# Kernel optimization log

Hardware: AMD Instinct MI355X
Metric: run time of the kernel (lower is better)

## Reference

```python
import jax, jax.numpy as jnp
import numpy as np

N_HEADS = 4

def layernorm(x, g, b):
    m = jnp.mean(x, -1, keepdims=True)
    v = jnp.var(x, -1, keepdims=True)
    return (x - m) / jnp.sqrt(v + 1e-5) * g + b

def conv1d(x, w, b, pad):
    y = jax.lax.conv_general_dilated(x, w, (1,), [(pad, pad)], dimension_numbers=('NCH', 'OIH', 'NCH'))
    return y + b[None, :, None]

def bn_eval(x, g, b, m, v):
    return (x - m[None, :, None]) / jnp.sqrt(v[None, :, None] + 1e-5) * g[None, :, None] + b[None, :, None]

def maxpool(x, k):
    return jax.lax.reduce_window(x, -jnp.inf, jax.lax.max, (1, 1, k), (1, 1, k), 'VALID')

def _forward(x, conv1_w, conv1_b, bn1_g, bn1_b, bn1_m, bn1_v, conv2_w, conv2_b, bn2_g, bn2_b, bn2_m, bn2_v, adj_prior, log_weights, gat_n1_g, gat_n1_b, gat_qkv_w, gat_qkv_b, gat_out_w, gat_out_b, gat_n2_g, gat_n2_b, gat_f1_w, gat_f1_b, gat_f2_w, gat_f2_b, gatn_g, gatn_b, gru_wih, gru_whh, gru_bih, gru_bhh, gate_w, gate_b):
    B, C, T = x.shape
    D = conv2_w.shape[0]
    dk = D // N_HEADS
    scale = dk ** -0.5
    # --- per-channel temporal CNN: (B,C,T) -> (B,C,T',D), T' = T//16 ---
    h = x.reshape(B * C, 1, T)
    h = maxpool(jax.nn.gelu(bn_eval(conv1d(h, conv1_w, conv1_b, 3), bn1_g, bn1_b, bn1_m, bn1_v), approximate=False), 4)
    h = maxpool(jax.nn.gelu(bn_eval(conv1d(h, conv2_w, conv2_b, 2), bn2_g, bn2_b, bn2_m, bn2_v), approximate=False), 4)
    Tp = h.shape[-1]
    h = jnp.transpose(h, (0, 2, 1)).reshape(B, C, Tp, D)
    # --- spectral dynamic adjacency ---
    h_avg = h.mean(axis=2)                                   # (B,C,D)
    hc = h_avg - h_avg.mean(-1, keepdims=True)
    hn = hc / (jnp.linalg.norm(hc, axis=-1, keepdims=True) + 1e-8)
    feat_corr = jnp.einsum('bcd,bed->bce', hn, hn)
    Xp = jnp.abs(jnp.fft.rfft(x, axis=-1))
    Xn = Xp / (jnp.linalg.norm(Xp, axis=-1, keepdims=True) + 1e-8)
    spec_coh = jnp.einsum('bcf,bef->bce', Xn, Xn)
    prior = (adj_prior + adj_prior.T)[None]
    w = jax.nn.softmax(log_weights)
    adj = w[0] * feat_corr + w[1] * spec_coh + w[2] * prior  # (B,C,C)
    # --- GAT stack over the C-node channel graph at every timestep ---
    ht = jnp.transpose(h, (0, 2, 1, 3)).reshape(B * Tp, C, D)
    adj_t = jnp.broadcast_to(adj[:, None], (B, Tp, C, C)).reshape(B * Tp, C, C)
    L = gat_qkv_w.shape[0]
    for l in range(L):
        hn1 = layernorm(ht, gat_n1_g[l], gat_n1_b[l])
        qkv = (hn1 @ gat_qkv_w[l].T + gat_qkv_b[l]).reshape(B * Tp, C, 3, N_HEADS, dk)
        q = jnp.moveaxis(qkv[:, :, 0], 1, 2)                 # (N,H,C,dk)
        k = jnp.moveaxis(qkv[:, :, 1], 1, 2)
        v = jnp.moveaxis(qkv[:, :, 2], 1, 2)
        attn = jnp.einsum('nhqd,nhkd->nhqk', q, k) * scale + adj_t[:, None]
        attn = jax.nn.softmax(attn, axis=-1)                 # dropout off (eval)
        out = jnp.einsum('nhqk,nhkd->nhqd', attn, v)
        out = jnp.moveaxis(out, 1, 2).reshape(B * Tp, C, D)
        ht = ht + out @ gat_out_w[l].T + gat_out_b[l]
        hn2 = layernorm(ht, gat_n2_g[l], gat_n2_b[l])
        ffn = jax.nn.gelu(hn2 @ gat_f1_w[l].T + gat_f1_b[l], approximate=False) @ gat_f2_w[l].T + gat_f2_b[l]
        ht = ht + ffn
    ht = layernorm(ht, gatn_g, gatn_b)
    hs = ht.reshape(B, Tp, C, D).transpose(0, 2, 1, 3).reshape(B * C, Tp, D)
    # --- bidirectional GRU (1 layer), final hidden states only ---
    G = gru_whh.shape[-1]
    def gru_last(xs, wih, whh, bih, bhh):
        def step(hprev, xt):
            gi = xt @ wih.T + bih
            gh = hprev @ whh.T + bhh
            ir, iz, inn = jnp.split(gi, 3, -1)
            hr, hz, hnn = jnp.split(gh, 3, -1)
            r = jax.nn.sigmoid(ir + hr)
            z = jax.nn.sigmoid(iz + hz)
            n = jnp.tanh(inn + r * hnn)
            hnew = (1.0 - z) * n + z * hprev
            return hnew, None
        h0 = jnp.zeros((xs.shape[0], G), xs.dtype)
        hl, _ = jax.lax.scan(step, h0, jnp.moveaxis(xs, 1, 0))
        return hl
    h_f = gru_last(hs, gru_wih[0], gru_whh[0], gru_bih[0], gru_bhh[0])
    h_b = gru_last(hs[:, ::-1], gru_wih[1], gru_whh[1], gru_bih[1], gru_bhh[1])
    h_out = jnp.concatenate([h_f, h_b], -1).reshape(B, C, 2 * G)
    # --- channel-attention readout ---
    gate = jax.nn.sigmoid(h_out @ gate_w.T + gate_b)         # (B,C,1)
    readout = (h_out * gate).sum(1) / (gate.sum(1) + 1e-8)   # (B,2G)
    return readout, adj, gate

def setup_inputs() -> dict:
    key = jax.random.key(0)
    ks = iter(jax.random.split(key, 64))
    B, C, T = 32, 16, 4096
    D, L, G = 64, 2, 64
    def rn(shape, s=0.08):
        return jax.random.normal(next(ks), shape, jnp.float32) * s
    return dict(
        x=jax.random.normal(next(ks), (B, C, T), jnp.float32),
        conv1_w=rn((32, 1, 7), 0.2), conv1_b=rn((32,)),
        bn1_g=jnp.ones((32,)), bn1_b=jnp.zeros((32,)), bn1_m=jnp.zeros((32,)), bn1_v=jnp.ones((32,)),
        conv2_w=rn((D, 32, 5), 0.1), conv2_b=rn((D,)),
        bn2_g=jnp.ones((D,)), bn2_b=jnp.zeros((D,)), bn2_m=jnp.zeros((D,)), bn2_v=jnp.ones((D,)),
        adj_prior=rn((C, C), 0.1), log_weights=jnp.zeros((3,)),
        gat_n1_g=jnp.ones((L, D)), gat_n1_b=jnp.zeros((L, D)),
        gat_qkv_w=rn((L, 3 * D, D)), gat_qkv_b=jnp.zeros((L, 3 * D)),
        gat_out_w=rn((L, D, D)), gat_out_b=jnp.zeros((L, D)),
        gat_n2_g=jnp.ones((L, D)), gat_n2_b=jnp.zeros((L, D)),
        gat_f1_w=rn((L, 2 * D, D)), gat_f1_b=jnp.zeros((L, 2 * D)),
        gat_f2_w=rn((L, D, 2 * D)), gat_f2_b=jnp.zeros((L, D)),
        gatn_g=jnp.ones((D,)), gatn_b=jnp.zeros((D,)),
        gru_wih=rn((2, 3 * G, D)), gru_whh=rn((2, 3 * G, G)),
        gru_bih=jnp.zeros((2, 3 * G)), gru_bhh=jnp.zeros((2, 3 * G)),
        gate_w=rn((1, 2 * G)), gate_b=jnp.zeros((1,)),
    )

def reference(x, conv1_w, conv1_b, bn1_g, bn1_b, bn1_m, bn1_v, conv2_w, conv2_b, bn2_g, bn2_b, bn2_m, bn2_v, adj_prior, log_weights, gat_n1_g, gat_n1_b, gat_qkv_w, gat_qkv_b, gat_out_w, gat_out_b, gat_n2_g, gat_n2_b, gat_f1_w, gat_f1_b, gat_f2_w, gat_f2_b, gatn_g, gatn_b, gru_wih, gru_whh, gru_bih, gru_bhh, gate_w, gate_b):
    return _forward(x, conv1_w, conv1_b, bn1_g, bn1_b, bn1_m, bn1_v, conv2_w, conv2_b, bn2_g, bn2_b, bn2_m, bn2_v, adj_prior, log_weights, gat_n1_g, gat_n1_b, gat_qkv_w, gat_qkv_b, gat_out_w, gat_out_b, gat_n2_g, gat_n2_b, gat_f1_w, gat_f1_b, gat_f2_w, gat_f2_b, gatn_g, gatn_b, gru_wih, gru_whh, gru_bih, gru_bhh, gate_w, gate_b)
```

## Files before the change

kernel.cpp:

```cpp
#include <hip/hip_runtime.h>
#include <hip/hip_bf16.h>
#include <math.h>

typedef __hip_bfloat16 bf16;
typedef unsigned short ushort_t;
typedef __attribute__((ext_vector_type(8))) short short8;
typedef __attribute__((ext_vector_type(4))) float f32x4;

__device__ __forceinline__ float b2f(bf16 v) { return __bfloat162float(v); }
__device__ __forceinline__ bf16 f2b(float v) { return __float2bfloat16(v); }
__device__ __forceinline__ float sigmoidf_(float x) { return 1.0f / (1.0f + __expf(-x)); }

__device__ __forceinline__ float geluf(float x) {
    float z = x * 0.70710678118654752f;
    float az = fabsf(z);
    float t = 1.0f / (1.0f + 0.3275911f * az);
    float poly = ((((1.061405429f * t - 1.453152027f) * t + 1.421413741f) * t
                   - 0.284496736f) * t + 0.254829592f) * t;
    float erfa = 1.0f - poly * __expf(-z * z);
    float er = (z < 0.f) ? -erfa : erfa;
    return 0.5f * x * (1.0f + er);
}

__device__ __forceinline__ unsigned pack2bf(float a, float b) {
    unsigned ua = __float_as_uint(a); ua = (ua + 0x7FFFu + ((ua >> 16) & 1u)) >> 16;
    unsigned ub = __float_as_uint(b); ub = (ub + 0x7FFFu + ((ub >> 16) & 1u)) >> 16;
    return ua | (ub << 16);
}
__device__ __forceinline__ ushort_t f2bu(float v) {
    unsigned u = __float_as_uint(v);
    u = (u + 0x7FFFu + ((u >> 16) & 1u)) >> 16;
    return (ushort_t)u;
}

__global__ __launch_bounds__(256) void k_detect(const unsigned* __restrict__ x, int* __restrict__ flag)
{
    __shared__ int cnt;
    if (threadIdx.x == 0) cnt = 0;
    __syncthreads();
    unsigned u = x[threadIdx.x] & 0xFFFFu;
    float f = __uint_as_float(u << 16);
    float a = fabsf(f);
    int sane = (f == 0.0f) || (a > 1e-8f && a < 1e4f);
    atomicAdd(&cnt, sane);
    __syncthreads();
    if (threadIdx.x == 0) *flag = (cnt >= 160) ? 1 : 0;
}

struct InPtrs { const void* p[35]; };
struct InOffs { int off[35]; int sz[35]; };

__global__ __launch_bounds__(256) void k_convert(InPtrs P, InOffs O, int total,
                                                 const int* __restrict__ flag,
                                                 float* __restrict__ cvt)
{
    int idx = blockIdx.x * 256 + threadIdx.x;
    if (idx >= total) return;
    int isb = *flag;
    float v = 0.f;
#pragma unroll 1
    for (int s = 0; s < 35; s++) {
        int rel = idx - O.off[s];
        if (rel >= 0 && rel < O.sz[s]) {
            v = isb ? b2f(((const bf16*)P.p[s])[rel]) : ((const float*)P.p[s])[rel];
            break;
        }
    }
    cvt[idx] = v;
}

__global__ __launch_bounds__(256) void k_pack(const float* __restrict__ qw, const float* __restrict__ ow,
                                              const float* __restrict__ f1w, const float* __restrict__ f2w,
                                              const float* __restrict__ gwih, const float* __restrict__ gwhh,
                                              const float* __restrict__ c2w,
                                              unsigned* __restrict__ dst)
{
    int i = blockIdx.x * 256 + threadIdx.x;
    if (i >= 62464) return;
    if (i >= 57344) {
        int j0 = (i - 57344) * 2;
        int tap = j0 >> 11, rem = j0 & 2047;
        int d = rem >> 5, ic = rem & 31;
        dst[i] = pack2bf(c2w[d * 160 + ic * 5 + tap], c2w[d * 160 + (ic + 1) * 5 + tap]);
        return;
    }
    const float* s; int rel;
    if (i < 12288)      { s = qw;   rel = i; }
    else if (i < 16384) { s = ow;   rel = i - 12288; }
    else if (i < 24576) { s = f1w;  rel = i - 16384; }
    else if (i < 32768) { s = f2w;  rel = i - 24576; }
    else if (i < 45056) { s = gwih; rel = i - 32768; }
    else                { s = gwhh; rel = i - 45056; }
    dst[i] = pack2bf(s[2 * rel], s[2 * rel + 1]);
}

__global__ __launch_bounds__(256) void k_front(
    const float* __restrict__ x,
    const float* __restrict__ c1w, const float* __restrict__ c1b,
    const float* __restrict__ bn1g, const float* __restrict__ bn1b, const float* __restrict__ bn1m, const float* __restrict__ bn1v,
    const float* __restrict__ c2b,
    const float* __restrict__ bn2g, const float* __restrict__ bn2b, const float* __restrict__ bn2m, const float* __restrict__ bn2v,
    const ushort_t* __restrict__ w2pk,
    float* __restrict__ h_main, float* __restrict__ Xn, float* __restrict__ hnf)
{
    __shared__ float smem[9984];
    int t = threadIdx.x;
    if (blockIdx.x >= 512) {
        float* re = smem;
        float* im = smem + 4096;
        float* red = smem + 8192;
        int bc = blockIdx.x - 512;
        const float* xr = x + (size_t)bc * 4096;
        for (int i = t; i < 4096; i += 256) {
            int r = __brev((unsigned)i) >> 20;
            re[r] = xr[i];
            im[r] = 0.f;
        }
        __syncthreads();
        for (int s = 1; s <= 12; s++) {
            int half = 1 << (s - 1);
            float ang = -6.283185307179586f / (float)(1 << s);
            for (int m = t; m < 2048; m += 256) {
                int j = m & (half - 1);
                int pos = ((m >> (s - 1)) << s) | j;
                float sn, cs;
                __sincosf(ang * (float)j, &sn, &cs);
                float ur = re[pos], ui = im[pos];
                float vr = re[pos + half], vi = im[pos + half];
                float tr = vr * cs - vi * sn;
                float ti = vr * sn + vi * cs;
                re[pos] = ur + tr; im[pos] = ui + ti;
                re[pos + half] = ur - tr; im[pos + half] = ui - ti;
            }
            __syncthreads();
        }
        float mag[9];
        float ss = 0.f;
        int cnt = 0;
        for (int f = t; f <= 2048; f += 256) {
            float m2 = re[f] * re[f] + im[f] * im[f];
            mag[cnt++] = sqrtf(m2);
            ss += m2;
        }
        for (int off = 32; off; off >>= 1) ss += __shfl_xor(ss, off, 64);
        if ((t & 63) == 0) red[t >> 6] = ss;
        __syncthreads();
        float tot = red[0] + red[1] + red[2] + red[3];
        float inv = 1.0f / (sqrtf(tot) + 1e-8f);
        cnt = 0;
        for (int f = t; f <= 2048; f += 256) Xn[(size_t)bc * 2049 + f] = mag[cnt++] * inv;
        return;
    }
    float* ubuf = smem;
    ushort_t* h1t = (ushort_t*)(smem + 4352);
    float* A2s = smem + 9552;
    float* B2s = smem + 9616;
    float* hsum = smem + 9680;
    int bc = blockIdx.x;
    int l = t & 63, w = t >> 6;
    int lo = l & 15, quad = l >> 4;

    if (t < 64) {
        float s = bn2g[t] * rsqrtf(bn2v[t] + 1e-5f);
        A2s[t] = s; B2s[t] = (c2b[t] - bn2m[t]) * s + bn2b[t];
    }
    int icp = t & 15;
    float w1r[2][7], A1r[2], B1r[2];
#pragma unroll
    for (int s = 0; s < 2; s++) {
        int ic = icp * 2 + s;
#pragma unroll
        for (int k = 0; k < 7; k++) w1r[s][k] = c1w[ic * 7 + k];
        float sc = bn1g[ic] * rsqrtf(bn1v[ic] + 1e-5f);
        A1r[s] = sc; B1r[s] = (c1b[ic] - bn1m[ic]) * sc + bn1b[ic];
    }
    short8 Afr[4][5];
#pragma unroll
    for (int dt = 0; dt < 4; dt++)
#pragma unroll
        for (int tap = 0; tap < 5; tap++)
            Afr[dt][tap] = *(const short8*)(w2pk + ((tap * 64 + dt * 16 + lo) * 32 + quad * 8));

    const float* xrow = x + (size_t)bc * 4096;
    float rs = 0.f;
    int dd = t & 63, pg = t >> 6;
    for (int tile = 0; tile < 4; tile++) {
        int X0 = 1024 * tile - 11;
        for (int i = t; i < 1056; i += 256) {
            int g = X0 + i;
            ubuf[i] = (g >= 0 && g < 4096) ? xrow[g] : 0.0f;
        }
        __syncthreads();
        for (int pos = (t >> 4); pos < 260; pos += 16) {
            const float4* xw = (const float4*)&ubuf[4 * pos];
            float4 fa = xw[0], fb = xw[1], fc = xw[2];
            float xv[12] = {fa.x, fa.y, fa.z, fa.w, fb.x, fb.y, fb.z, fb.w,
                            fc.x, fc.y, fc.z, fc.w};
            int t1pg = tile * 256 + pos - 2;
            bool ok = (t1pg >= 0 && t1pg < 1024);
            float res[2];
#pragma unroll
            for (int s = 0; s < 2; s++) {
                float a0 = 0.f, a1 = 0.f, a2 = 0.f, a3 = 0.f;
#pragma unroll
                for (int k = 0; k < 7; k++) {
                    float wv = w1r[s][k];
                    a0 += xv[k] * wv;     a1 += xv[k + 1] * wv;
                    a2 += xv[k + 2] * wv; a3 += xv[k + 3] * wv;
                }
                float A = A1r[s], B = B1r[s];
                a0 = a0 * A + B; a1 = a1 * A + B; a2 = a2 * A + B; a3 = a3 * A + B;
                float mx = fmaxf(fmaxf(a0, a1), fmaxf(a2, a3));
                float mn = fminf(fminf(a0, a1), fminf(a2, a3));
                res[s] = ok ? fmaxf(geluf(mx), geluf(mn)) : 0.0f;
            }
            ((unsigned*)h1t)[pos * 20 + icp] = pack2bf(res[0], res[1]);
        }
        __syncthreads();
        float* houtile = ubuf;
#pragma unroll
        for (int ni = 0; ni < 4; ni++) {
            int nt = w * 4 + ni;
            short8 bfr[5];
#pragma unroll
            for (int tap = 0; tap < 5; tap++)
                bfr[tap] = *(const short8*)&h1t[(nt * 16 + lo + tap) * 40 + quad * 8];
#pragma unroll
            for (int dt = 0; dt < 4; dt++) {
                f32x4 acc = {0.f, 0.f, 0.f, 0.f};
#pragma unroll
                for (int tap = 0; tap < 5; tap++)
                    acc = __builtin_amdgcn_mfma_f32_16x16x32_bf16(Afr[dt][tap], bfr[tap], acc, 0, 0, 0);
                const float4 a2 = *(const float4*)&A2s[dt * 16 + quad * 4];
                const float4 b2 = *(const float4*)&B2s[dt * 16 + quad * 4];
                float a2a[4] = {a2.x, a2.y, a2.z, a2.w};
                float b2a[4] = {b2.x, b2.y, b2.z, b2.w};
#pragma unroll
                for (int r = 0; r < 4; r++) {
                    float v = acc[r] * a2a[r] + b2a[r];
                    float o1 = __shfl_xor(v, 1);
                    float mx = fmaxf(v, o1), mn = fminf(v, o1);
                    float mx2 = __shfl_xor(mx, 2), mn2 = __shfl_xor(mn, 2);
                    mx = fmaxf(mx, mx2); mn = fminf(mn, mn2);
                    float res = fmaxf(geluf(mx), geluf(mn));
                    if ((lo & 3) == 0)
                        houtile[(nt * 4 + (lo >> 2)) * 68 + dt * 16 + quad * 4 + r] = res;
                }
            }
        }
        __syncthreads();
#pragma unroll
        for (int i = 0; i < 16; i++) rs += ubuf[(pg * 16 + i) * 68 + dd];
        float* dst = h_main + (size_t)bc * 16384 + tile * 4096;
        for (int i = t * 4; i < 4096; i += 1024) {
            float4 v = *(const float4*)&ubuf[(i >> 6) * 68 + (i & 63)];
            *(float4*)&dst[i] = v;
        }
        __syncthreads();
    }
    hsum[t] = rs;
    __syncthreads();
    if (t < 64) {
        float avg = (hsum[t] + hsum[64 + t] + hsum[128 + t] + hsum[192 + t]) * (1.0f / 256.0f);
        float tot = avg;
        for (int off = 32; off; off >>= 1) tot += __shfl_xor(tot, off, 64);
        float hc = avg - tot * (1.0f / 64.0f);
        float sq = hc * hc;
        for (int off = 32; off; off >>= 1) sq += __shfl_xor(sq, off, 64);
        hnf[bc * 64 + t] = hc / (sqrtf(sq) + 1e-8f);
    }
}

__global__ __launch_bounds__(256) void k_adj(
    const float* __restrict__ Xn, const float* __restrict__ hnf,
    const float* __restrict__ prior, const float* __restrict__ logw,
    float* __restrict__ adjw, void* __restrict__ out, const int* __restrict__ flag)
{
    __shared__ float xt[16][257];
    __shared__ float hh[16 * 64];
    int b = blockIdx.x, t = threadIdx.x;
    int c = t >> 4, e = t & 15;
    for (int i = t; i < 1024; i += 256) hh[i] = hnf[b * 1024 + i];
    __syncthreads();
    float fc = 0.f;
    for (int d = 0; d < 64; d++) fc += hh[c * 64 + d] * hh[e * 64 + d];
    float sc = 0.f;
    const float* Xb = Xn + (size_t)b * 16 * 2049;
    for (int f0 = 0; f0 < 2048; f0 += 256) {
        __syncthreads();
        for (int i = t; i < 16 * 256; i += 256) {
            int rr = i >> 8, ff = i & 255;
            xt[rr][ff] = Xb[rr * 2049 + f0 + ff];
        }
        __syncthreads();
        for (int ff = 0; ff < 256; ff++) sc += xt[c][ff] * xt[e][ff];
    }
    sc += Xb[c * 2049 + 2048] * Xb[e * 2049 + 2048];
    float l0 = logw[0], l1 = logw[1], l2 = logw[2];
    float mx = fmaxf(l0, fmaxf(l1, l2));
    float e0 = __expf(l0 - mx), e1 = __expf(l1 - mx), e2 = __expf(l2 - mx);
    float isum = 1.0f / (e0 + e1 + e2);
    float pr = prior[c * 16 + e] + prior[e * 16 + c];
    float v = (e0 * fc + e1 * sc + e2 * pr) * isum;
    adjw[b * 256 + t] = v;
    if (*flag) ((bf16*)out)[4096 + b * 256 + t] = f2b(v);
    else       ((float*)out)[4096 + b * 256 + t] = v;
}

__device__ __forceinline__ void ln_wave(const float (*ht)[68], ushort_t (*out)[72],
                                        const float* __restrict__ g, const float* __restrict__ bp,
                                        int quad, int lo)
{
    float v[16];
    const float4* row = (const float4*)(&ht[lo][quad * 16]);
#pragma unroll
    for (int i = 0; i < 4; i++) {
        float4 a = row[i];
        v[4 * i] = a.x; v[4 * i + 1] = a.y; v[4 * i + 2] = a.z; v[4 * i + 3] = a.w;
    }
    float s = 0.f;
#pragma unroll
    for (int i = 0; i < 16; i++) s += v[i];
    s += __shfl_xor(s, 16); s += __shfl_xor(s, 32);
    float mean = s * (1.0f / 64.0f);
    float q = 0.f;
#pragma unroll
    for (int i = 0; i < 16; i++) { float d = v[i] - mean; q += d * d; }
    q += __shfl_xor(q, 16); q += __shfl_xor(q, 32);
    float rstd = rsqrtf(q * (1.0f / 64.0f) + 1e-5f);
    const float4* gp = (const float4*)(g + quad * 16);
    const float4* bb4 = (const float4*)(bp + quad * 16);
    unsigned* orow = (unsigned*)(&out[lo][quad * 16]);
#pragma unroll
    for (int i = 0; i < 4; i++) {
        float4 gg = gp[i], bb = bb4[i];
        float o0 = (v[4 * i] - mean) * rstd * gg.x + bb.x;
        float o1 = (v[4 * i + 1] - mean) * rstd * gg.y + bb.y;
        float o2 = (v[4 * i + 2] - mean) * rstd * gg.z + bb.z;
        float o3 = (v[4 * i + 3] - mean) * rstd * gg.w + bb.w;
        orow[2 * i] = pack2bf(o0, o1);
        orow[2 * i + 1] = pack2bf(o2, o3);
    }
}

__global__ __launch_bounds__(256) void k_gat(
    const float* __restrict__ hm, const float* __restrict__ adjw,
    const ushort_t* __restrict__ wpk,
    const float* __restrict__ qb_, const float* __restrict__ ob_,
    const float* __restrict__ f1b_, const float* __restrict__ f2b_,
    const float* __restrict__ n1g_, const float* __restrict__ n1b_,
    const float* __restrict__ n2g_, const float* __restrict__ n2b_,
    const float* __restrict__ gng, const float* __restrict__ gnb,
    ushort_t* __restrict__ hmb)
{
    __shared__ float htw_all[4][16][68];
    __shared__ ushort_t hnw_all[4][16][72];
    __shared__ ushort_t qkb_all[4][16][200];
    __shared__ ushort_t pb_all[4][16][72];
    __shared__ ushort_t vt_all[4][64][24];
    int t = threadIdx.x;
    int w = t >> 6, l = t & 63;
    int quad = l >> 4, lo = l & 15;
    int n = blockIdx.x * 4 + w;
    int b = n >> 8, tp = n & 255;
    float (*htw)[68] = htw_all[w];
    ushort_t (*hnw)[72] = hnw_all[w];
    ushort_t (*qkb)[200] = qkb_all[w];
    ushort_t (*pb)[72] = pb_all[w];
    ushort_t (*vt)[24] = vt_all[w];
    const float* src = hm + (size_t)b * 16 * 16384 + (size_t)tp * 64;
#pragma unroll
    for (int c = 0; c < 16; c++) htw[c][l] = src[(size_t)c * 16384 + l];
    float adjr[4];
#pragma unroll
    for (int r = 0; r < 4; r++) adjr[r] = adjw[b * 256 + (quad * 4 + r) * 16 + lo];

    for (int layer = 0; layer < 2; layer++) {
        const ushort_t* wq  = wpk + layer * 12288;
        const ushort_t* wo  = wpk + 24576 + layer * 4096;
        const ushort_t* wf1 = wpk + 32768 + layer * 8192;
        const ushort_t* wf2 = wpk + 49152 + layer * 8192;
        const float* qb = qb_ + layer * 192;
        const float* ob = ob_ + layer * 64;
        const float* f1b = f1b_ + layer * 128;
        const float* f2b = f2b_ + layer * 64;

        ln_wave(htw, hnw, n1g_ + layer * 64, n1b_ + layer * 64, quad, lo);

        short8 a0 = *(const short8*)&hnw[lo][quad * 8];
        short8 a1 = *(const short8*)&hnw[lo][32 + quad * 8];
#pragma unroll
        for (int nt = 0; nt < 12; nt++) {
            const ushort_t* wr = wq + (nt * 16 + lo) * 64 + quad * 8;
            short8 b0 = *(const short8*)wr;
            short8 b1 = *(const short8*)(wr + 32);
            f32x4 acc = {0.f, 0.f, 0.f, 0.f};
            acc = __builtin_amdgcn_mfma_f32_16x16x32_bf16(a0, b0, acc, 0, 0, 0);
            acc = __builtin_amdgcn_mfma_f32_16x16x32_bf16(a1, b1, acc, 0, 0, 0);
            float bias = qb[nt * 16 + lo];
            if (nt < 8) {
#pragma unroll
                for (int r = 0; r < 4; r++) qkb[quad * 4 + r][nt * 16 + lo] = f2bu(acc[r] + bias);
            } else {
#pragma unroll
                for (int r = 0; r < 4; r++) vt[(nt - 8) * 16 + lo][quad * 4 + r] = f2bu(acc[r] + bias);
            }
        }

        short8 zf = {0, 0, 0, 0, 0, 0, 0, 0};
#pragma unroll
        for (int h = 0; h < 4; h++) {
            short8 qf = zf, kf = zf;
            if (quad < 2) {
                qf = *(const short8*)&qkb[lo][h * 16 + quad * 8];
                kf = *(const short8*)&qkb[lo][64 + h * 16 + quad * 8];
            }
            f32x4 s4 = {0.f, 0.f, 0.f, 0.f};
            s4 = __builtin_amdgcn_mfma_f32_16x16x32_bf16(qf, kf, s4, 0, 0, 0);
#pragma unroll
            for (int r = 0; r < 4; r++) {
                float sv = s4[r] * 0.25f + adjr[r];
                float mx = sv;
                mx = fmaxf(mx, __shfl_xor(mx, 1));
                mx = fmaxf(mx, __shfl_xor(mx, 2));
                mx = fmaxf(mx, __shfl_xor(mx, 4));
                mx = fmaxf(mx, __shfl_xor(mx, 8));
                float e = __expf(sv - mx);
                float sm = e;
                sm += __shfl_xor(sm, 1);
                sm += __shfl_xor(sm, 2);
                sm += __shfl_xor(sm, 4);
                sm += __shfl_xor(sm, 8);
                pb[quad * 4 + r][h * 16 + lo] = f2bu(e / sm);
            }
        }
#pragma unroll
        for (int h = 0; h < 4; h++) {
            short8 pf = zf, vf = zf;
            if (quad < 2) {
                pf = *(const short8*)&pb[lo][h * 16 + quad * 8];
                vf = *(const short8*)&vt[h * 16 + lo][quad * 8];
            }
            f32x4 oc = {0.f, 0.f, 0.f, 0.f};
            oc = __builtin_amdgcn_mfma_f32_16x16x32_bf16(pf, vf, oc, 0, 0, 0);
#pragma unroll
            for (int r = 0; r < 4; r++) qkb[quad * 4 + r][h * 16 + lo] = f2bu(oc[r]);
        }
        short8 pa0 = *(const short8*)&qkb[lo][quad * 8];
        short8 pa1 = *(const short8*)&qkb[lo][32 + quad * 8];
#pragma unroll
        for (int nt = 0; nt < 4; nt++) {
            const ushort_t* wr = wo + (nt * 16 + lo) * 64 + quad * 8;
            short8 b0 = *(const short8*)wr;
            short8 b1 = *(const short8*)(wr + 32);
            f32x4 acc = {0.f, 0.f, 0.f, 0.f};
            acc = __builtin_amdgcn_mfma_f32_16x16x32_bf16(pa0, b0, acc, 0, 0, 0);
            acc = __builtin_amdgcn_mfma_f32_16x16x32_bf16(pa1, b1, acc, 0, 0, 0);
            float bias = ob[nt * 16 + lo];
#pragma unroll
            for (int r = 0; r < 4; r++) htw[quad * 4 + r][nt * 16 + lo] += acc[r] + bias;
        }
        ln_wave(htw, hnw, n2g_ + layer * 64, n2b_ + layer * 64, quad, lo);
        short8 fa0 = *(const short8*)&hnw[lo][quad * 8];
        short8 fa1 = *(const short8*)&hnw[lo][32 + quad * 8];
#pragma unroll
        for (int nt = 0; nt < 8; nt++) {
            const ushort_t* wr = wf1 + (nt * 16 + lo) * 64 + quad * 8;
            short8 b0 = *(const short8*)wr;
            short8 b1 = *(const short8*)(wr + 32);
            f32x4 acc = {0.f, 0.f, 0.f, 0.f};
            acc = __builtin_amdgcn_mfma_f32_16x16x32_bf16(fa0, b0, acc, 0, 0, 0);
            acc = __builtin_amdgcn_mfma_f32_16x16x32_bf16(fa1, b1, acc, 0, 0, 0);
            float bias = f1b[nt * 16 + lo];
#pragma unroll
            for (int r = 0; r < 4; r++) qkb[quad * 4 + r][nt * 16 + lo] = f2bu(geluf(acc[r] + bias));
        }
        short8 ga[4];
#pragma unroll
        for (int kb = 0; kb < 4; kb++) ga[kb] = *(const short8*)&qkb[lo][kb * 32 + quad * 8];
#pragma unroll
        for (int nt = 0; nt < 4; nt++) {
            const ushort_t* wr = wf2 + (nt * 16 + lo) * 128 + quad * 8;
            f32x4 acc = {0.f, 0.f, 0.f, 0.f};
#pragma unroll
            for (int kb = 0; kb < 4; kb++) {
                short8 bb = *(const short8*)(wr + kb * 32);
                acc = __builtin_amdgcn_mfma_f32_16x16x32_bf16(ga[kb], bb, acc, 0, 0, 0);
            }
            float bias = f2b[nt * 16 + lo];
#pragma unroll
            for (int r = 0; r < 4; r++) htw[quad * 4 + r][nt * 16 + lo] += acc[r] + bias;
        }
    }
    {
        float v[16];
        const float4* row = (const float4*)(&htw[lo][quad * 16]);
#pragma unroll
        for (int i = 0; i < 4; i++) {
            float4 a = row[i];
            v[4 * i] = a.x; v[4 * i + 1] = a.y; v[4 * i + 2] = a.z; v[4 * i + 3] = a.w;
        }
        float s = 0.f;
#pragma unroll
        for (int i = 0; i < 16; i++) s += v[i];
        s += __shfl_xor(s, 16); s += __shfl_xor(s, 32);
        float mean = s * (1.0f / 64.0f);
        float q = 0.f;
#pragma unroll
        for (int i = 0; i < 16; i++) { float d = v[i] - mean; q += d * d; }
        q += __shfl_xor(q, 16); q += __shfl_xor(q, 32);
        float rstd = rsqrtf(q * (1.0f / 64.0f) + 1e-5f);
        const float4* gp = (const float4*)(gng + quad * 16);
        const float4* bb4 = (const float4*)(gnb + quad * 16);
        unsigned u[8];
#pragma unroll
        for (int i = 0; i < 4; i++) {
            float4 gg = gp[i], bb = bb4[i];
            float o0 = (v[4 * i] - mean) * rstd * gg.x + bb.x;
            float o1 = (v[4 * i + 1] - mean) * rstd * gg.y + bb.y;
            float o2 = (v[4 * i + 2] - mean) * rstd * gg.z + bb.z;
            float o3 = (v[4 * i + 3] - mean) * rstd * gg.w + bb.w;
            u[2 * i] = pack2bf(o0, o1);
            u[2 * i + 1] = pack2bf(o2, o3);
        }
        ushort_t* dst = hmb + (size_t)(b * 16 + lo) * 16384 + (size_t)tp * 64 + quad * 16;
        ((uint4*)dst)[0] = make_uint4(u[0], u[1], u[2], u[3]);
        ((uint4*)dst)[1] = make_uint4(u[4], u[5], u[6], u[7]);
    }
}

__global__ __launch_bounds__(256) void k_gru(
    const ushort_t* __restrict__ hmb, const ushort_t* __restrict__ wgru,
    const float* __restrict__ bih_, const float* __restrict__ bhh_,
    float* __restrict__ h_out)
{
    __shared__ ushort_t hbuf[2][16][72];
    int t = threadIdx.x;
    int w = t >> 6, l = t & 63;
    int lo = l & 15, qd = l >> 4;
    int dir = blockIdx.x >> 5;
    int cseq0 = (blockIdx.x & 31) * 16;
    const ushort_t* wih = wgru + dir * 12288;
    const ushort_t* whh = wgru + 24576 + dir * 12288;
    const ushort_t* pr0 = wih + ((w) * 16 + lo) * 64 + qd * 8;
    const ushort_t* pz0 = wih + ((4 + w) * 16 + lo) * 64 + qd * 8;
    const ushort_t* pn0 = wih + ((8 + w) * 16 + lo) * 64 + qd * 8;
    const ushort_t* hr0 = whh + ((w) * 16 + lo) * 64 + qd * 8;
    const ushort_t* hz0 = whh + ((4 + w) * 16 + lo) * 64 + qd * 8;
    const ushort_t* hn0 = whh + ((8 + w) * 16 + lo) * 64 + qd * 8;
    short8 wi_r0 = *(const short8*)pr0, wi_r1 = *(const short8*)(pr0 + 32);
    short8 wi_z0 = *(const short8*)pz0, wi_z1 = *(const short8*)(pz0 + 32);
    short8 wi_n0 = *(const short8*)pn0, wi_n1 = *(const short8*)(pn0 + 32);
    short8 wh_r0 = *(const short8*)hr0, wh_r1 = *(const short8*)(hr0 + 32);
    short8 wh_z0 = *(const short8*)hz0, wh_z1 = *(const short8*)(hz0 + 32);
    short8 wh_n0 = *(const short8*)hn0, wh_n1 = *(const short8*)(hn0 + 32);
    int d_base = w * 16 + qd * 4;
    float bsr[4], bsz[4], bin[4], bhn[4];
#pragma unroll
    for (int r = 0; r < 4; r++) {
        bsr[r] = bih_[dir * 192 + d_base + r] + bhh_[dir * 192 + d_base + r];
        bsz[r] = bih_[dir * 192 + 64 + d_base + r] + bhh_[dir * 192 + 64 + d_base + r];
        bin[r] = bih_[dir * 192 + 128 + d_base + r];
        bhn[r] = bhh_[dir * 192 + 128 + d_base + r];
    }
    const ushort_t* xrow = hmb + (size_t)(cseq0 + lo) * 16384 + qd * 8;
    for (int i = t; i < 2 * 16 * 72; i += 256) ((ushort_t*)hbuf)[i] = 0;
    float h_old[4] = {0.f, 0.f, 0.f, 0.f};

    int s0 = dir ? 255 : 0;
    int s1 = dir ? 254 : 1;
    int s2 = dir ? 253 : 2;
    short8 xc0 = *(const short8*)(xrow + s0 * 64);
    short8 xc1 = *(const short8*)(xrow + s0 * 64 + 32);
    short8 xA0 = *(const short8*)(xrow + s1 * 64);
    short8 xA1 = *(const short8*)(xrow + s1 * 64 + 32);
    short8 xB0 = *(const short8*)(xrow + s2 * 64);
    short8 xB1 = *(const short8*)(xrow + s2 * 64 + 32);
    f32x4 axr = {0.f, 0.f, 0.f, 0.f}, axz = {0.f, 0.f, 0.f, 0.f}, axn = {0.f, 0.f, 0.f, 0.f};
    axr = __builtin_amdgcn_mfma_f32_16x16x32_bf16(wi_r0, xc0, axr, 0, 0, 0);
    axr = __builtin_amdgcn_mfma_f32_16x16x32_bf16(wi_r1, xc1, axr, 0, 0, 0);
    axz = __builtin_amdgcn_mfma_f32_16x16x32_bf16(wi_z0, xc0, axz, 0, 0, 0);
    axz = __builtin_amdgcn_mfma_f32_16x16x32_bf16(wi_z1, xc1, axz, 0, 0, 0);
    axn = __builtin_amdgcn_mfma_f32_16x16x32_bf16(wi_n0, xc0, axn, 0, 0, 0);
    axn = __builtin_amdgcn_mfma_f32_16x16x32_bf16(wi_n1, xc1, axn, 0, 0, 0);
    __syncthreads();
#pragma unroll 2
    for (int step = 0; step < 256; step++) {
        int cur = step & 1, nxt = cur ^ 1;
        f32x4 nxr = {0.f, 0.f, 0.f, 0.f}, nxz = {0.f, 0.f, 0.f, 0.f}, nxn = {0.f, 0.f, 0.f, 0.f};
        nxr = __builtin_amdgcn_mfma_f32_16x16x32_bf16(wi_r0, xA0, nxr, 0, 0, 0);
        nxr = __builtin_amdgcn_mfma_f32_16x16x32_bf16(wi_r1, xA1, nxr, 0, 0, 0);
        nxz = __builtin_amdgcn_mfma_f32_16x16x32_bf16(wi_z0, xA0, nxz, 0, 0, 0);
        nxz = __builtin_amdgcn_mfma_f32_16x16x32_bf16(wi_z1, xA1, nxz, 0, 0, 0);
        nxn = __builtin_amdgcn_mfma_f32_16x16x32_bf16(wi_n0, xA0, nxn, 0, 0, 0);
        nxn = __builtin_amdgcn_mfma_f32_16x16x32_bf16(wi_n1, xA1, nxn, 0, 0, 0);
        xA0 = xB0; xA1 = xB1;
        int tl = step + 3 > 255 ? 255 : step + 3;
        int sf = dir ? 255 - tl : tl;
        xB0 = *(const short8*)(xrow + sf * 64);
        xB1 = *(const short8*)(xrow + sf * 64 + 32);
        short8 bh0 = *(const short8*)&hbuf[cur][lo][qd * 8];
        short8 bh1 = *(const short8*)&hbuf[cur][lo][32 + qd * 8];
        f32x4 ar = axr, az = axz;
        f32x4 anh = {0.f, 0.f, 0.f, 0.f};
        ar = __builtin_amdgcn_mfma_f32_16x16x32_bf16(wh_r0, bh0, ar, 0, 0, 0);
        ar = __builtin_amdgcn_mfma_f32_16x16x32_bf16(wh_r1, bh1, ar, 0, 0, 0);
        az = __builtin_amdgcn_mfma_f32_16x16x32_bf16(wh_z0, bh0, az, 0, 0, 0);
        az = __builtin_amdgcn_mfma_f32_16x16x32_bf16(wh_z1, bh1, az, 0, 0, 0);
        anh = __builtin_amdgcn_mfma_f32_16x16x32_bf16(wh_n0, bh0, anh, 0, 0, 0);
        anh = __builtin_amdgcn_mfma_f32_16x16x32_bf16(wh_n1, bh1, anh, 0, 0, 0);
        float hv[4];
#pragma unroll
        for (int r = 0; r < 4; r++) {
            float gr = sigmoidf_(ar[r] + bsr[r]);
            float gz = sigmoidf_(az[r] + bsz[r]);
            float nin = (axn[r] + bin[r]) + gr * (anh[r] + bhn[r]);
            nin = fminf(fmaxf(nin, -15.f), 15.f);
            float e = __expf(-2.f * nin);
            float gn = (1.f - e) / (1.f + e);
            float hn = gn + gz * (h_old[r] - gn);
            h_old[r] = hn;
            hv[r] = hn;
        }
        *(uint2*)&hbuf[nxt][lo][d_base] = make_uint2(pack2bf(hv[0], hv[1]), pack2bf(hv[2], hv[3]));
        asm volatile("s_waitcnt lgkmcnt(0)\n\ts_barrier" ::: "memory");
        axr = nxr; axz = nxz; axn = nxn;
    }
    *(float4*)&h_out[(size_t)(cseq0 + lo) * 128 + dir * 64 + d_base] =
        make_float4(h_old[0], h_old[1], h_old[2], h_old[3]);
}

__global__ __launch_bounds__(128) void k_readout(
    const float* __restrict__ h_out, const float* __restrict__ gw, const float* __restrict__ gb,
    void* __restrict__ out, const int* __restrict__ flag)
{
    __shared__ float gate_s[16];
    __shared__ float gws[128];
    int b = blockIdx.x, t = threadIdx.x;
    gws[t] = gw[t];
    __syncthreads();
    int isb = *flag;
    if (t < 16) {
        const float* hr = h_out + (size_t)(b * 16 + t) * 128;
        float acc = gb[0];
        for (int k = 0; k < 128; k++) acc += hr[k] * gws[k];
        float g = sigmoidf_(acc);
        gate_s[t] = g;
        if (isb) ((bf16*)out)[12288 + b * 16 + t] = f2b(g);
        else     ((float*)out)[12288 + b * 16 + t] = g;
    }
    __syncthreads();
    float den = 1e-8f;
#pragma unroll
    for (int c = 0; c < 16; c++) den += gate_s[c];
    float num = 0.f;
#pragma unroll
    for (int c = 0; c < 16; c++) num += h_out[(size_t)(b * 16 + c) * 128 + t] * gate_s[c];
    float v = num / den;
    if (isb) ((bf16*)out)[b * 128 + t] = f2b(v);
    else     ((float*)out)[b * 128 + t] = v;
}

extern "C" void kernel_launch(void* const* d_in, const int* in_sizes, int n_in,
                              void* d_out, int out_size, void* d_ws, size_t ws_size,
                              hipStream_t stream)
{
    int* flag = (int*)d_ws;
    float* cvt = (float*)((char*)d_ws + 256);

    InPtrs P;
    InOffs O;
    int cum = 0;
    for (int i = 0; i < 35; i++) {
        P.p[i] = d_in[i];
        O.off[i] = cum;
        O.sz[i] = in_sizes[i];
        cum += (in_sizes[i] + 7) & ~7;
    }
    int total = cum;

    const float* x     = cvt + O.off[0];
    const float* c1w   = cvt + O.off[1];
    const float* c1b   = cvt + O.off[2];
    const float* bn1g  = cvt + O.off[3];
    const float* bn1b  = cvt + O.off[4];
    const float* bn1m  = cvt + O.off[5];
    const float* bn1v  = cvt + O.off[6];
    const float* c2w   = cvt + O.off[7];
    const float* c2b   = cvt + O.off[8];
    const float* bn2g  = cvt + O.off[9];
    const float* bn2b  = cvt + O.off[10];
    const float* bn2m  = cvt + O.off[11];
    const float* bn2v  = cvt + O.off[12];
    const float* prior = cvt + O.off[13];
    const float* logw  = cvt + O.off[14];
    const float* n1g   = cvt + O.off[15];
    const float* n1b   = cvt + O.off[16];
    const float* qkvw  = cvt + O.off[17];
    const float* qkvb  = cvt + O.off[18];
    const float* outw  = cvt + O.off[19];
    const float* outb  = cvt + O.off[20];
    const float* n2g   = cvt + O.off[21];
    const float* n2b   = cvt + O.off[22];
    const float* f1w   = cvt + O.off[23];
    const float* f1b   = cvt + O.off[24];
    const float* f2w   = cvt + O.off[25];
    const float* f2b_  = cvt + O.off[26];
    const float* gng   = cvt + O.off[27];
    const float* gnb   = cvt + O.off[28];
    const float* gwih  = cvt + O.off[29];
    const float* gwhh  = cvt + O.off[30];
    const float* gbih  = cvt + O.off[31];
    const float* gbhh  = cvt + O.off[32];
    const float* gatew = cvt + O.off[33];
    const float* gateb = cvt + O.off[34];

    float* fbase = cvt + ((total + 63) & ~63);
    float* hm   = fbase;
    float* Xn   = hm + 8388608;
    float* hnf  = Xn + 1049088;
    float* adjw = hnf + 32768;
    float* hout = adjw + 8192;
    unsigned* wpk = (unsigned*)(hout + 65536);
    ushort_t* hmb = (ushort_t*)(wpk + 62464);

    k_detect<<<1, 256, 0, stream>>>((const unsigned*)d_in[0], flag);
    k_convert<<<(total + 255) / 256, 256, 0, stream>>>(P, O, total, flag, cvt);
    k_pack<<<244, 256, 0, stream>>>(qkvw, outw, f1w, f2w, gwih, gwhh, c2w, wpk);
    k_front<<<1024, 256, 0, stream>>>(x, c1w, c1b, bn1g, bn1b, bn1m, bn1v,
                                      c2b, bn2g, bn2b, bn2m, bn2v,
                                      (const ushort_t*)(wpk + 57344), hm, Xn, hnf);
    k_adj<<<32, 256, 0, stream>>>(Xn, hnf, prior, logw, adjw, d_out, flag);
    k_gat<<<2048, 256, 0, stream>>>(hm, adjw, (const ushort_t*)wpk,
                                    qkvb, outb, f1b, f2b_, n1g, n1b, n2g, n2b, gng, gnb, hmb);
    k_gru<<<64, 256, 0, stream>>>(hmb, (const ushort_t*)(wpk + 32768), gbih, gbhh, hout);
    k_readout<<<32, 128, 0, stream>>>(hout, gatew, gateb, d_out, flag);
}
```

Before: 652.4 us.

## Pack two real FFTs per block, store spectra in bf16, use MFMA for coherence

The spectral branch now computes two channels' real FFTs with one complex FFT, placing one signal in the real part and one in the imaginary part and separating them through conjugate symmetry. This halves the FFT blocks from 512 to 256. Normalized magnitudes are written as padded bf16 rows, and k_adj computes the 16x16 spectral coherence Gram matrix with bf16 MFMA instructions instead of a scalar shared-memory loop. This cuts FFT work, memory traffic and the serial dot-product cost, at the price of bf16 rounding in spec_coh.

```diff
diff --git a/kernel.cpp b/kernel.cpp
--- a/kernel.cpp
+++ b/kernel.cpp
@@ -101,7 +101,7 @@
     const float* __restrict__ c2b,
     const float* __restrict__ bn2g, const float* __restrict__ bn2b, const float* __restrict__ bn2m, const float* __restrict__ bn2v,
     const ushort_t* __restrict__ w2pk,
-    float* __restrict__ h_main, float* __restrict__ Xn, float* __restrict__ hnf)
+    float* __restrict__ h_main, ushort_t* __restrict__ Xnb, float* __restrict__ hnf)
 {
     __shared__ float smem[9984];
     int t = threadIdx.x;
@@ -109,12 +109,14 @@
         float* re = smem;
         float* im = smem + 4096;
         float* red = smem + 8192;
-        int bc = blockIdx.x - 512;
-        const float* xr = x + (size_t)bc * 4096;
+        int bc2 = blockIdx.x - 512;
+        int b = bc2 >> 3, cp = bc2 & 7;
+        const float* xa = x + ((size_t)b * 16 + 2 * cp) * 4096;
+        const float* xb = xa + 4096;
         for (int i = t; i < 4096; i += 256) {
             int r = __brev((unsigned)i) >> 20;
-            re[r] = xr[i];
-            im[r] = 0.f;
+            re[r] = xa[i];
+            im[r] = xb[i];
         }
         __syncthreads();
         for (int s = 1; s <= 12; s++) {
@@ -134,21 +136,40 @@
             }
             __syncthreads();
         }
-        float mag[9];
-        float ss = 0.f;
-        int cnt = 0;
-        for (int f = t; f <= 2048; f += 256) {
-            float m2 = re[f] * re[f] + im[f] * im[f];
-            mag[cnt++] = sqrtf(m2);
-            ss += m2;
-        }
-        for (int off = 32; off; off >>= 1) ss += __shfl_xor(ss, off, 64);
-        if ((t & 63) == 0) red[t >> 6] = ss;
+        float maga[9], magb[9];
+        float ssa = 0.f, ssb = 0.f;
+#pragma unroll
+        for (int it = 0; it < 9; it++) {
+            int k = t + it * 256;
+            float ma = 0.f, mb = 0.f;
+            if (k <= 2048) {
+                int kn = (4096 - k) & 4095;
+                float Rk = re[k], Ik = im[k], Rn = re[kn], In = im[kn];
+                float ra = 0.5f * (Rk + Rn), ia = 0.5f * (Ik - In);
+                float rb = 0.5f * (Ik + In), ib = 0.5f * (Rn - Rk);
+                ma = sqrtf(ra * ra + ia * ia);
+                mb = sqrtf(rb * rb + ib * ib);
+                ssa += ma * ma; ssb += mb * mb;
+            }
+            maga[it] = ma; magb[it] = mb;
+        }
+        for (int off = 32; off; off >>= 1) { ssa += __shfl_xor(ssa, off, 64); ssb += __shfl_xor(ssb, off, 64); }
+        int w = t >> 6;
+        if ((t & 63) == 0) { red[w] = ssa; red[4 + w] = ssb; }
         __syncthreads();
-        float tot = red[0] + red[1] + red[2] + red[3];
-        float inv = 1.0f / (sqrtf(tot) + 1e-8f);
-        cnt = 0;
-        for (int f = t; f <= 2048; f += 256) Xn[(size_t)bc * 2049 + f] = mag[cnt++] * inv;
+        float inva = 1.0f / (sqrtf(red[0] + red[1] + red[2] + red[3]) + 1e-8f);
+        float invb = 1.0f / (sqrtf(red[4] + red[5] + red[6] + red[7]) + 1e-8f);
+        ushort_t* rowa = Xnb + ((size_t)b * 16 + 2 * cp) * 2080;
+        ushort_t* rowb = rowa + 2080;
+#pragma unroll
+        for (int it = 0; it < 9; it++) {
+            int k = t + it * 256;
+            if (k <= 2048) {
+                rowa[k] = f2bu(maga[it] * inva);
+                rowb[k] = f2bu(magb[it] * invb);
+            }
+        }
+        for (int f = 2049 + t; f < 2080; f += 256) { rowa[f] = 0; rowb[f] = 0; }
         return;
     }
     float* ubuf = smem;
@@ -272,30 +293,30 @@
 }
 
 __global__ __launch_bounds__(256) void k_adj(
-    const float* __restrict__ Xn, const float* __restrict__ hnf,
+    const ushort_t* __restrict__ Xnb, const float* __restrict__ hnf,
     const float* __restrict__ prior, const float* __restrict__ logw,
     float* __restrict__ adjw, void* __restrict__ out, const int* __restrict__ flag)
 {
-    __shared__ float xt[16][257];
-    __shared__ float hh[16 * 64];
+    __shared__ float tile[4][16][17];
+    __shared__ float hh[1024];
     int b = blockIdx.x, t = threadIdx.x;
+    int w = t >> 6, l = t & 63;
+    int lo = l & 15, quad = l >> 4;
+    for (int i = t; i < 1024; i += 256) hh[i] = hnf[b * 1024 + i];
+    const ushort_t* base = Xnb + (size_t)b * 16 * 2080 + lo * 2080 + quad * 8;
+    f32x4 acc = {0.f, 0.f, 0.f, 0.f};
+    for (int kb = w; kb < 65; kb += 4) {
+        short8 f = *(const short8*)(base + kb * 32);
+        acc = __builtin_amdgcn_mfma_f32_16x16x32_bf16(f, f, acc, 0, 0, 0);
+    }
+#pragma unroll
+    for (int r = 0; r < 4; r++) tile[w][quad * 4 + r][lo] = acc[r];
+    __syncthreads();
     int c = t >> 4, e = t & 15;
-    for (int i = t; i < 1024; i += 256) hh[i] = hnf[b * 1024 + i];
-    __syncthreads();
+    float sc = tile[0][c][e] + tile[1][c][e] + tile[2][c][e] + tile[3][c][e];
     float fc = 0.f;
+#pragma unroll
     for (int d = 0; d < 64; d++) fc += hh[c * 64 + d] * hh[e * 64 + d];
-    float sc = 0.f;
-    const float* Xb = Xn + (size_t)b * 16 * 2049;
-    for (int f0 = 0; f0 < 2048; f0 += 256) {
-        __syncthreads();
-        for (int i = t; i < 16 * 256; i += 256) {
-            int rr = i >> 8, ff = i & 255;
-            xt[rr][ff] = Xb[rr * 2049 + f0 + ff];
-        }
-        __syncthreads();
-        for (int ff = 0; ff < 256; ff++) sc += xt[c][ff] * xt[e][ff];
-    }
-    sc += Xb[c * 2049 + 2048] * Xb[e * 2049 + 2048];
     float l0 = logw[0], l1 = logw[1], l2 = logw[2];
     float mx = fmaxf(l0, fmaxf(l1, l2));
     float e0 = __expf(l0 - mx), e1 = __expf(l1 - mx), e2 = __expf(l2 - mx);
@@ -716,21 +737,21 @@
     const float* gateb = cvt + O.off[34];
 
     float* fbase = cvt + ((total + 63) & ~63);
-    float* hm   = fbase;
-    float* Xn   = hm + 8388608;
-    float* hnf  = Xn + 1049088;
-    float* adjw = hnf + 32768;
-    float* hout = adjw + 8192;
+    float* hm    = fbase;
+    ushort_t* Xnb = (ushort_t*)(hm + 8388608);
+    float* hnf   = fbase + 8921088;
+    float* adjw  = hnf + 32768;
+    float* hout  = adjw + 8192;
     unsigned* wpk = (unsigned*)(hout + 65536);
     ushort_t* hmb = (ushort_t*)(wpk + 62464);
 
     k_detect<<<1, 256, 0, stream>>>((const unsigned*)d_in[0], flag);
     k_convert<<<(total + 255) / 256, 256, 0, stream>>>(P, O, total, flag, cvt);
     k_pack<<<244, 256, 0, stream>>>(qkvw, outw, f1w, f2w, gwih, gwhh, c2w, wpk);
-    k_front<<<1024, 256, 0, stream>>>(x, c1w, c1b, bn1g, bn1b, bn1m, bn1v,
-                                      c2b, bn2g, bn2b, bn2m, bn2v,
-                                      (const ushort_t*)(wpk + 57344), hm, Xn, hnf);
-    k_adj<<<32, 256, 0, stream>>>(Xn, hnf, prior, logw, adjw, d_out, flag);
+    k_front<<<768, 256, 0, stream>>>(x, c1w, c1b, bn1g, bn1b, bn1m, bn1v,
+                                     c2b, bn2g, bn2b, bn2m, bn2v,
+                                     (const ushort_t*)(wpk + 57344), hm, Xnb, hnf);
+    k_adj<<<32, 256, 0, stream>>>(Xnb, hnf, prior, logw, adjw, d_out, flag);
     k_gat<<<2048, 256, 0, stream>>>(hm, adjw, (const ushort_t*)wpk,
                                     qkvb, outb, f1b, f2b_, n1g, n1b, n2g, n2b, gng, gnb, hmb);
     k_gru<<<64, 256, 0, stream>>>(hmb, (const ushort_t*)(wpk + 32768), gbih, gbhh, hout);
```

After: 603.1 us. -7.5%, faster.
